# Performance work log

Hardware: AMD Instinct MI355X
Metric: run time of the kernel (lower is better)

The kernel has to match this reference:

```python
import jax, jax.numpy as jnp
import numpy as np

N_NODES = 50000
NODE_IN = 128
EDGE_IN = 16
HIDDEN = 128
N_MP = 800000
N_PRED = 400000


def setup_inputs() -> dict:
    key = jax.random.key(0)
    ks = jax.random.split(key, 12)
    s = lambda fan_in: 1.0 / np.sqrt(fan_in)
    inp = {
        'x': jax.random.normal(ks[0], (N_NODES, NODE_IN), jnp.float32),
        'mp_edge_index': jax.random.randint(ks[1], (2, N_MP), 0, N_NODES, jnp.int64),
        'pred_edge_index': jax.random.randint(ks[2], (2, N_PRED), 0, N_NODES, jnp.int64),
        'pred_edge_attr': jax.random.normal(ks[3], (N_PRED, EDGE_IN), jnp.float32),
        # SAGEConv1: lin_l (neighbors, with bias), lin_r (root, no bias)
        'W1_l': jax.random.normal(ks[4], (HIDDEN, NODE_IN), jnp.float32) * s(NODE_IN),
        'b1': jnp.zeros((HIDDEN,), jnp.float32),
        'W1_r': jax.random.normal(ks[5], (HIDDEN, NODE_IN), jnp.float32) * s(NODE_IN),
        # SAGEConv2
        'W2_l': jax.random.normal(ks[6], (HIDDEN, HIDDEN), jnp.float32) * s(HIDDEN),
        'b2': jnp.zeros((HIDDEN,), jnp.float32),
        'W2_r': jax.random.normal(ks[7], (HIDDEN, HIDDEN), jnp.float32) * s(HIDDEN),
        # edge MLP: Linear(2*H+E -> H), ReLU, Linear(H -> 1)
        'Wm1': jax.random.normal(ks[8], (HIDDEN, 2 * HIDDEN + EDGE_IN), jnp.float32) * s(2 * HIDDEN + EDGE_IN),
        'bm1': jnp.zeros((HIDDEN,), jnp.float32),
        'Wm2': jax.random.normal(ks[9], (1, HIDDEN), jnp.float32) * s(HIDDEN),
        'bm2': jnp.zeros((1,), jnp.float32),
    }
    return inp


def _sage_conv(h, src, dst, W_l, b_l, W_r, n_nodes):
    # PyG SAGEConv with mean aggregation: out_i = W_l @ mean_{j->i} h_j + b_l + W_r @ h_i
    msg_sum = jax.ops.segment_sum(h[src], dst, num_segments=n_nodes)
    deg = jax.ops.segment_sum(jnp.ones((src.shape[0],), h.dtype), dst, num_segments=n_nodes)
    mean = msg_sum / jnp.maximum(deg, 1.0)[:, None]
    return mean @ W_l.T + b_l + h @ W_r.T


def reference(x, mp_edge_index, pred_edge_index, pred_edge_attr,
              W1_l, b1, W1_r, W2_l, b2, W2_r, Wm1, bm1, Wm2, bm2):
    n = x.shape[0]
    src, dst = mp_edge_index[0], mp_edge_index[1]
    h = jax.nn.relu(_sage_conv(x, src, dst, W1_l, b1, W1_r, n))
    h = jax.nn.relu(_sage_conv(h, src, dst, W2_l, b2, W2_r, n))
    ps, pd = pred_edge_index[0], pred_edge_index[1]
    edge_repr = jnp.concatenate([h[ps], h[pd], pred_edge_attr], axis=-1)  # [E_pred, 2H+E]
    hidden = jax.nn.relu(edge_repr @ Wm1.T + bm1)
    return (hidden @ Wm2.T + bm2)[:, 0]
```

## Files before the change

kernel.cpp:

```cpp
#include <hip/hip_runtime.h>
#include <hip/hip_bf16.h>

#define HIDDEN 128

typedef __attribute__((ext_vector_type(8))) short s16x8;
typedef __attribute__((ext_vector_type(4))) short s16x4;
typedef __attribute__((ext_vector_type(4))) float f32x4;
typedef __attribute__((ext_vector_type(8))) __bf16 bf16x8;

__device__ __forceinline__ short f2bf(float x) {
    unsigned u = __float_as_uint(x);
    unsigned r = (u + 0x7fffu + ((u >> 16) & 1u)) >> 16;
    return (short)r;
}
__device__ __forceinline__ float bf2f(short s) {
    return __uint_as_float(((unsigned)(unsigned short)s) << 16);
}

__global__ void k_split(const float* __restrict__ in, short* __restrict__ hi,
                        short* __restrict__ lo, int n4) {
    int i = blockIdx.x * blockDim.x + threadIdx.x;
    if (i >= n4) return;
    float4 v = ((const float4*)in)[i];
    s16x4 h, l;
    h[0] = f2bf(v.x); l[0] = f2bf(v.x - bf2f(h[0]));
    h[1] = f2bf(v.y); l[1] = f2bf(v.y - bf2f(h[1]));
    h[2] = f2bf(v.z); l[2] = f2bf(v.z - bf2f(h[2]));
    h[3] = f2bf(v.w); l[3] = f2bf(v.w - bf2f(h[3]));
    ((s16x4*)hi)[i] = h;
    ((s16x4*)lo)[i] = l;
}

__global__ void k_packw_conv(const float* __restrict__ Wl, const float* __restrict__ Wr,
                             short* __restrict__ Bh, short* __restrict__ Bl) {
    int idx = blockIdx.x * blockDim.x + threadIdx.x;
    if (idx >= 8 * 8 * 64) return;
    int l = idx & 63;
    int t = (idx >> 6) & 7;
    int s = idx >> 9;
    int n = t * 16 + (l & 15);
    int kbase = s * 32 + (l >> 4) * 8;
    s16x8 h, lo;
    #pragma unroll
    for (int j = 0; j < 8; ++j) {
        int k = kbase + j;
        float v = (k < 128) ? Wl[n * 128 + k] : Wr[n * 128 + (k - 128)];
        short hs = f2bf(v);
        h[j] = hs;
        lo[j] = f2bf(v - bf2f(hs));
    }
    ((s16x8*)Bh)[idx] = h;
    ((s16x8*)Bl)[idx] = lo;
}

__global__ void k_packw_uv(const float* __restrict__ Wm1, short* __restrict__ Bh,
                           short* __restrict__ Bl) {
    int idx = blockIdx.x * blockDim.x + threadIdx.x;
    if (idx >= 4 * 16 * 64) return;
    int l = idx & 63;
    int t = (idx >> 6) & 15;
    int s = idx >> 10;
    int np = t * 16 + (l & 15);
    int kbase = s * 32 + (l >> 4) * 8;
    s16x8 h, lo;
    #pragma unroll
    for (int j = 0; j < 8; ++j) {
        int k = kbase + j;
        float v = (np < 128) ? Wm1[np * 272 + k] : Wm1[(np - 128) * 272 + 128 + k];
        short hs = f2bf(v);
        h[j] = hs;
        lo[j] = f2bf(v - bf2f(hs));
    }
    ((s16x8*)Bh)[idx] = h;
    ((s16x8*)Bl)[idx] = lo;
}

__global__ void k_deg(const int* __restrict__ dst, int* __restrict__ deg, int n_edges) {
    for (int e = blockIdx.x * blockDim.x + threadIdx.x; e < n_edges; e += gridDim.x * blockDim.x)
        atomicAdd(&deg[dst[e]], 1);
}

__global__ __launch_bounds__(1024) void k_scan_blk(const int* __restrict__ deg,
                                                   int* __restrict__ row_start,
                                                   int* __restrict__ part, int n) {
    __shared__ int wsum[16];
    int tid = threadIdx.x;
    int lane = tid & 63;
    int w = tid >> 6;
    int i = blockIdx.x * 1024 + tid;
    int v = (i < n) ? deg[i] : 0;
    int s = v;
    #pragma unroll
    for (int off = 1; off < 64; off <<= 1) {
        int t = __shfl_up(s, off, 64);
        if (lane >= off) s += t;
    }
    if (lane == 63) wsum[w] = s;
    __syncthreads();
    if (w == 0) {
        int ws = (lane < 16) ? wsum[lane] : 0;
        #pragma unroll
        for (int off = 1; off < 16; off <<= 1) {
            int t = __shfl_up(ws, off, 64);
            if (lane >= off) ws += t;
        }
        if (lane < 16) wsum[lane] = ws;
    }
    __syncthreads();
    int incl = s + ((w > 0) ? wsum[w - 1] : 0);
    if (i < n) row_start[i] = incl - v;
    if (tid == 1023) part[blockIdx.x] = incl;
}

__global__ void k_scan_top(int* __restrict__ part, int* __restrict__ row_start,
                           int P, int n) {
    int lane = threadIdx.x;
    int v = (lane < P) ? part[lane] : 0;
    int s = v;
    #pragma unroll
    for (int off = 1; off < 64; off <<= 1) {
        int t = __shfl_up(s, off, 64);
        if (lane >= off) s += t;
    }
    if (lane < P) part[lane] = s - v;
    if (lane == P - 1) row_start[n] = s;
}

__global__ __launch_bounds__(1024) void k_scan_add(int* __restrict__ row_start,
                                                   int* __restrict__ cursor,
                                                   const int* __restrict__ part, int n) {
    int i = blockIdx.x * 1024 + threadIdx.x;
    if (i < n) {
        int r = row_start[i] + part[blockIdx.x];
        row_start[i] = r;
        cursor[i] = r;
    }
}

__global__ void k_fill(const int* __restrict__ src, const int* __restrict__ dst,
                       int* __restrict__ cursor, int* __restrict__ csr, int n_edges) {
    for (int e = blockIdx.x * blockDim.x + threadIdx.x; e < n_edges; e += gridDim.x * blockDim.x) {
        int d = dst[e];
        int p = atomicAdd(&cursor[d], 1);
        csr[p] = src[e];
    }
}

__global__ __launch_bounds__(256) void k_agg_f32(const float* __restrict__ feat,
                                                 const int* __restrict__ row_start,
                                                 const int* __restrict__ csr,
                                                 short* __restrict__ Mh,
                                                 short* __restrict__ Ml, int n_nodes) {
    int wave = (blockIdx.x * 256 + threadIdx.x) >> 6;
    if (wave >= n_nodes) return;
    int lane = threadIdx.x & 63;
    int s = row_start[wave], e = row_start[wave + 1];
    const float2* f2p = (const float2*)feat;
    float ax = 0.f, ay = 0.f;
    for (int j = s; j < e; ++j) {
        int nb = csr[j];
        float2 v = f2p[nb * 64 + lane];
        ax += v.x; ay += v.y;
    }
    float inv = (e > s) ? 1.0f / (float)(e - s) : 0.0f;
    float m0 = ax * inv, m1 = ay * inv;
    short h0 = f2bf(m0), l0 = f2bf(m0 - bf2f(h0));
    short h1 = f2bf(m1), l1 = f2bf(m1 - bf2f(h1));
    ((ushort2*)Mh)[wave * 64 + lane] = make_ushort2((unsigned short)h0, (unsigned short)h1);
    ((ushort2*)Ml)[wave * 64 + lane] = make_ushort2((unsigned short)l0, (unsigned short)l1);
}

__global__ __launch_bounds__(256) void k_agg_sp(const short* __restrict__ Fh,
                                                const short* __restrict__ Fl,
                                                const int* __restrict__ row_start,
                                                const int* __restrict__ csr,
                                                short* __restrict__ Mh,
                                                short* __restrict__ Ml, int n_nodes) {
    int wave = (blockIdx.x * 256 + threadIdx.x) >> 6;
    if (wave >= n_nodes) return;
    int lane = threadIdx.x & 63;
    int s = row_start[wave], e = row_start[wave + 1];
    const ushort2* fh = (const ushort2*)Fh;
    const ushort2* fl = (const ushort2*)Fl;
    float ax = 0.f, ay = 0.f;
    for (int j = s; j < e; ++j) {
        int nb = csr[j];
        ushort2 qh = fh[nb * 64 + lane];
        ushort2 ql = fl[nb * 64 + lane];
        ax += bf2f((short)qh.x) + bf2f((short)ql.x);
        ay += bf2f((short)qh.y) + bf2f((short)ql.y);
    }
    float inv = (e > s) ? 1.0f / (float)(e - s) : 0.0f;
    float m0 = ax * inv, m1 = ay * inv;
    short h0 = f2bf(m0), l0 = f2bf(m0 - bf2f(h0));
    short h1 = f2bf(m1), l1 = f2bf(m1 - bf2f(h1));
    ((ushort2*)Mh)[wave * 64 + lane] = make_ushort2((unsigned short)h0, (unsigned short)h1);
    ((ushort2*)Ml)[wave * 64 + lane] = make_ushort2((unsigned short)l0, (unsigned short)l1);
}

__global__ __launch_bounds__(256, 4) void k_convm(
    const short* __restrict__ Mh, const short* __restrict__ Ml,
    const short* __restrict__ Rh, const short* __restrict__ Rl,
    const short* __restrict__ Bh, const short* __restrict__ Bl,
    const float* __restrict__ bias, short* __restrict__ Oh, short* __restrict__ Ol,
    int n_nodes) {
    __shared__ __align__(16) short Ah[32][264];
    __shared__ __align__(16) short Al[32][264];
    int tid = threadIdx.x;
    int node0 = blockIdx.x * 32;
    const s16x8* Mh8 = (const s16x8*)Mh;
    const s16x8* Ml8 = (const s16x8*)Ml;
    const s16x8* Rh8 = (const s16x8*)Rh;
    const s16x8* Rl8 = (const s16x8*)Rl;
    for (int i = tid; i < 32 * 32; i += 256) {
        int row = i >> 5, grp = i & 31;
        int node = node0 + row;
        s16x8 vh = (s16x8)0, vl = (s16x8)0;
        if (node < n_nodes) {
            vh = (grp < 16) ? Mh8[node * 16 + grp] : Rh8[node * 16 + (grp - 16)];
            vl = (grp < 16) ? Ml8[node * 16 + grp] : Rl8[node * 16 + (grp - 16)];
        }
        *(s16x8*)&Ah[row][grp * 8] = vh;
        *(s16x8*)&Al[row][grp * 8] = vl;
    }
    __syncthreads();

    int lane = tid & 63;
    int w = tid >> 6;
    int rowid = lane & 15;
    int g = lane >> 4;
    int t0 = w * 2;

    f32x4 acc[2][2];
    acc[0][0] = (f32x4)0.f; acc[0][1] = (f32x4)0.f;
    acc[1][0] = (f32x4)0.f; acc[1][1] = (f32x4)0.f;

    const bf16x8* Bh8 = (const bf16x8*)Bh;
    const bf16x8* Bl8 = (const bf16x8*)Bl;
    bf16x8 bh0 = Bh8[t0 * 64 + lane];
    bf16x8 bh1 = Bh8[(t0 + 1) * 64 + lane];
    bf16x8 bl0 = Bl8[t0 * 64 + lane];
    bf16x8 bl1 = Bl8[(t0 + 1) * 64 + lane];

    #pragma unroll
    for (int s = 0; s < 8; ++s) {
        bf16x8 nh0 = bh0, nh1 = bh1, nl0 = bl0, nl1 = bl1;
        if (s < 7) {
            nh0 = Bh8[((s + 1) * 8 + t0) * 64 + lane];
            nh1 = Bh8[((s + 1) * 8 + t0 + 1) * 64 + lane];
            nl0 = Bl8[((s + 1) * 8 + t0) * 64 + lane];
            nl1 = Bl8[((s + 1) * 8 + t0 + 1) * 64 + lane];
        }
        int kf = s * 32 + g * 8;
        bf16x8 a_h[2], a_l[2];
        #pragma unroll
        for (int m = 0; m < 2; ++m) {
            a_h[m] = *(const bf16x8*)&Ah[m * 16 + rowid][kf];
            a_l[m] = *(const bf16x8*)&Al[m * 16 + rowid][kf];
        }
        #pragma unroll
        for (int m = 0; m < 2; ++m) {
            acc[m][0] = __builtin_amdgcn_mfma_f32_16x16x32_bf16(a_h[m], bh0, acc[m][0], 0, 0, 0);
            acc[m][1] = __builtin_amdgcn_mfma_f32_16x16x32_bf16(a_h[m], bh1, acc[m][1], 0, 0, 0);
            acc[m][0] = __builtin_amdgcn_mfma_f32_16x16x32_bf16(a_l[m], bh0, acc[m][0], 0, 0, 0);
            acc[m][1] = __builtin_amdgcn_mfma_f32_16x16x32_bf16(a_l[m], bh1, acc[m][1], 0, 0, 0);
            acc[m][0] = __builtin_amdgcn_mfma_f32_16x16x32_bf16(a_h[m], bl0, acc[m][0], 0, 0, 0);
            acc[m][1] = __builtin_amdgcn_mfma_f32_16x16x32_bf16(a_h[m], bl1, acc[m][1], 0, 0, 0);
        }
        bh0 = nh0; bh1 = nh1; bl0 = nl0; bl1 = nl1;
    }

    int n0 = w * 32 + rowid;
    int n1 = n0 + 16;
    float b_0 = bias[n0], b_1 = bias[n1];
    unsigned short* OhU = (unsigned short*)Oh;
    unsigned short* OlU = (unsigned short*)Ol;
    #pragma unroll
    for (int m = 0; m < 2; ++m) {
        int node = node0 + m * 16 + g * 4;
        #pragma unroll
        for (int r = 0; r < 4; ++r) {
            if (node + r < n_nodes) {
                float v0 = fmaxf(acc[m][0][r] + b_0, 0.f);
                float v1 = fmaxf(acc[m][1][r] + b_1, 0.f);
                short h0 = f2bf(v0), l0 = f2bf(v0 - bf2f(h0));
                short h1 = f2bf(v1), l1 = f2bf(v1 - bf2f(h1));
                OhU[(node + r) * 128 + n0] = (unsigned short)h0;
                OlU[(node + r) * 128 + n0] = (unsigned short)l0;
                OhU[(node + r) * 128 + n1] = (unsigned short)h1;
                OlU[(node + r) * 128 + n1] = (unsigned short)l1;
            }
        }
    }
}

__global__ __launch_bounds__(256, 4) void k_guv(
    const short* __restrict__ H2h, const short* __restrict__ H2l,
    const short* __restrict__ Bh, const short* __restrict__ Bl,
    float* __restrict__ U, float* __restrict__ V, int n_nodes) {
    __shared__ __align__(16) short Ah[32][136];
    __shared__ __align__(16) short Al[32][136];
    int tid = threadIdx.x;
    int node0 = blockIdx.x * 32;
    const s16x8* Hh8 = (const s16x8*)H2h;
    const s16x8* Hl8 = (const s16x8*)H2l;
    for (int i = tid; i < 32 * 16; i += 256) {
        int row = i >> 4, grp = i & 15;
        int node = node0 + row;
        s16x8 vh = (s16x8)0, vl = (s16x8)0;
        if (node < n_nodes) {
            vh = Hh8[node * 16 + grp];
            vl = Hl8[node * 16 + grp];
        }
        *(s16x8*)&Ah[row][grp * 8] = vh;
        *(s16x8*)&Al[row][grp * 8] = vl;
    }
    __syncthreads();

    int lane = tid & 63;
    int w = tid >> 6;
    int rowid = lane & 15;
    int g = lane >> 4;
    int t0 = w * 4;

    f32x4 acc[2][4];
    #pragma unroll
    for (int m = 0; m < 2; ++m)
        #pragma unroll
        for (int q = 0; q < 4; ++q) acc[m][q] = (f32x4)0.f;

    const bf16x8* Bh8 = (const bf16x8*)Bh;
    const bf16x8* Bl8 = (const bf16x8*)Bl;

    #pragma unroll
    for (int s = 0; s < 4; ++s) {
        bf16x8 bh[4], bl[4];
        #pragma unroll
        for (int q = 0; q < 4; ++q) {
            bh[q] = Bh8[(s * 16 + t0 + q) * 64 + lane];
            bl[q] = Bl8[(s * 16 + t0 + q) * 64 + lane];
        }
        int kf = s * 32 + g * 8;
        bf16x8 a_h[2], a_l[2];
        #pragma unroll
        for (int m = 0; m < 2; ++m) {
            a_h[m] = *(const bf16x8*)&Ah[m * 16 + rowid][kf];
            a_l[m] = *(const bf16x8*)&Al[m * 16 + rowid][kf];
        }
        #pragma unroll
        for (int m = 0; m < 2; ++m) {
            #pragma unroll
            for (int q = 0; q < 4; ++q) {
                acc[m][q] = __builtin_amdgcn_mfma_f32_16x16x32_bf16(a_h[m], bh[q], acc[m][q], 0, 0, 0);
                acc[m][q] = __builtin_amdgcn_mfma_f32_16x16x32_bf16(a_l[m], bh[q], acc[m][q], 0, 0, 0);
                acc[m][q] = __builtin_amdgcn_mfma_f32_16x16x32_bf16(a_h[m], bl[q], acc[m][q], 0, 0, 0);
            }
        }
    }

    float* dstbase = (w < 2) ? U : V;
    int cb = (w & 1) * 64 + rowid;
    #pragma unroll
    for (int m = 0; m < 2; ++m) {
        int node = node0 + m * 16 + g * 4;
        #pragma unroll
        for (int q = 0; q < 4; ++q) {
            int col = cb + q * 16;
            #pragma unroll
            for (int r = 0; r < 4; ++r) {
                if (node + r < n_nodes)
                    dstbase[(node + r) * 128 + col] = acc[m][q][r];
            }
        }
    }
}

__global__ __launch_bounds__(256) void k_edge(
    const float* __restrict__ U, const float* __restrict__ V,
    const int* __restrict__ ps, const int* __restrict__ pd,
    const float* __restrict__ attr, const float* __restrict__ Wm1,
    const float* __restrict__ bm1, const float* __restrict__ wm2,
    const float* __restrict__ bm2, float* __restrict__ outp, int n_edges) {
    int lane = threadIdx.x & 63;
    int wid = (blockIdx.x * 256 + threadIdx.x) >> 6;
    int nw = (gridDim.x * 256) >> 6;

    int j0 = 2 * lane;
    float wa0[16], wa1[16];
    #pragma unroll
    for (int k4 = 0; k4 < 4; ++k4) {
        float4 t = *(const float4*)&Wm1[j0 * 272 + 256 + k4 * 4];
        wa0[k4 * 4 + 0] = t.x; wa0[k4 * 4 + 1] = t.y; wa0[k4 * 4 + 2] = t.z; wa0[k4 * 4 + 3] = t.w;
        float4 u = *(const float4*)&Wm1[(j0 + 1) * 272 + 256 + k4 * 4];
        wa1[k4 * 4 + 0] = u.x; wa1[k4 * 4 + 1] = u.y; wa1[k4 * 4 + 2] = u.z; wa1[k4 * 4 + 3] = u.w;
    }
    float bb0 = bm1[j0], bb1 = bm1[j0 + 1];
    float wm0 = wm2[j0], wm1v = wm2[j0 + 1];
    float bm2v = bm2[0];

    const float2* U2 = (const float2*)U;
    const float2* V2 = (const float2*)V;
    const float4* at4 = (const float4*)attr;

    for (int e = wid; e < n_edges; e += nw) {
        int s = ps[e];
        int d = pd[e];
        float2 u = U2[s * 64 + lane];
        float2 v = V2[d * 64 + lane];
        float4 a0 = at4[e * 4 + 0];
        float4 a1 = at4[e * 4 + 1];
        float4 a2 = at4[e * 4 + 2];
        float4 a3 = at4[e * 4 + 3];
        float av[16] = {a0.x, a0.y, a0.z, a0.w, a1.x, a1.y, a1.z, a1.w,
                        a2.x, a2.y, a2.z, a2.w, a3.x, a3.y, a3.z, a3.w};
        float t0 = 0.f, t1 = 0.f;
        #pragma unroll
        for (int k = 0; k < 16; ++k) {
            t0 += wa0[k] * av[k];
            t1 += wa1[k] * av[k];
        }
        float p = fmaxf(u.x + v.x + t0 + bb0, 0.f) * wm0
                + fmaxf(u.y + v.y + t1 + bb1, 0.f) * wm1v;
        p += __shfl_xor(p, 32, 64);
        p += __shfl_xor(p, 16, 64);
        p += __shfl_xor(p, 8, 64);
        p += __shfl_xor(p, 4, 64);
        p += __shfl_xor(p, 2, 64);
        p += __shfl_xor(p, 1, 64);
        if (lane == 0) outp[e] = p + bm2v;
    }
}

extern "C" void kernel_launch(void* const* d_in, const int* in_sizes, int n_in,
                              void* d_out, int out_size, void* d_ws, size_t ws_size,
                              hipStream_t stream) {
    const float* x     = (const float*)d_in[0];
    const int*   mp    = (const int*)d_in[1];
    const int*   pe    = (const int*)d_in[2];
    const float* attr  = (const float*)d_in[3];
    const float* W1_l  = (const float*)d_in[4];
    const float* b1    = (const float*)d_in[5];
    const float* W1_r  = (const float*)d_in[6];
    const float* W2_l  = (const float*)d_in[7];
    const float* b2    = (const float*)d_in[8];
    const float* W2_r  = (const float*)d_in[9];
    const float* Wm1   = (const float*)d_in[10];
    const float* bm1   = (const float*)d_in[11];
    const float* Wm2   = (const float*)d_in[12];
    const float* bm2   = (const float*)d_in[13];
    float* out = (float*)d_out;

    const int n_nodes = in_sizes[0] / HIDDEN;
    const int n_mp    = in_sizes[1] / 2;
    const int n_pred  = in_sizes[2] / 2;

    const int* mp_src = mp;
    const int* mp_dst = mp + n_mp;
    const int* p_src  = pe;
    const int* p_dst  = pe + n_pred;

    char* ws = (char*)d_ws;
    size_t off = 0;
    auto alloc = [&](size_t bytes) -> void* {
        void* p = ws + off;
        off += (bytes + 255) & ~(size_t)255;
        return p;
    };
    short* Wc1h = (short*)alloc(8 * 8 * 64 * 8 * sizeof(short));
    short* Wc1l = (short*)alloc(8 * 8 * 64 * 8 * sizeof(short));
    short* Wc2h = (short*)alloc(8 * 8 * 64 * 8 * sizeof(short));
    short* Wc2l = (short*)alloc(8 * 8 * 64 * 8 * sizeof(short));
    short* Buvh = (short*)alloc(4 * 16 * 64 * 8 * sizeof(short));
    short* Buvl = (short*)alloc(4 * 16 * 64 * 8 * sizeof(short));
    int*   deg    = (int*)alloc((size_t)n_nodes * sizeof(int));
    int*   rowst  = (int*)alloc(((size_t)n_nodes + 1) * sizeof(int));
    int*   cursor = (int*)alloc((size_t)n_nodes * sizeof(int));
    int*   part   = (int*)alloc(64 * sizeof(int));
    int*   csr    = (int*)alloc((size_t)n_mp * sizeof(int));
    short* Xh  = (short*)alloc((size_t)n_nodes * HIDDEN * sizeof(short));
    short* Xl  = (short*)alloc((size_t)n_nodes * HIDDEN * sizeof(short));
    short* Mh  = (short*)alloc((size_t)n_nodes * HIDDEN * sizeof(short));
    short* Ml  = (short*)alloc((size_t)n_nodes * HIDDEN * sizeof(short));
    short* H1h = (short*)alloc((size_t)n_nodes * HIDDEN * sizeof(short));
    short* H1l = (short*)alloc((size_t)n_nodes * HIDDEN * sizeof(short));
    short* H2h = (short*)alloc((size_t)n_nodes * HIDDEN * sizeof(short));
    short* H2l = (short*)alloc((size_t)n_nodes * HIDDEN * sizeof(short));
    float* Ubuf = (float*)alloc((size_t)n_nodes * HIDDEN * sizeof(float));
    float* Vbuf = (float*)alloc((size_t)n_nodes * HIDDEN * sizeof(float));
    (void)ws_size; (void)n_in; (void)out_size;

    const int P = (n_nodes + 1023) / 1024;

    hipMemsetAsync(deg, 0, (size_t)n_nodes * sizeof(int), stream);

    k_packw_conv<<<16, 256, 0, stream>>>(W1_l, W1_r, Wc1h, Wc1l);
    k_packw_conv<<<16, 256, 0, stream>>>(W2_l, W2_r, Wc2h, Wc2l);
    k_packw_uv<<<16, 256, 0, stream>>>(Wm1, Buvh, Buvl);
    k_split<<<(n_nodes * 32 + 255) / 256, 256, 0, stream>>>(x, Xh, Xl, n_nodes * 32);

    k_deg<<<(n_mp + 255) / 256, 256, 0, stream>>>(mp_dst, deg, n_mp);
    k_scan_blk<<<P, 1024, 0, stream>>>(deg, rowst, part, n_nodes);
    k_scan_top<<<1, 64, 0, stream>>>(part, rowst, P, n_nodes);
    k_scan_add<<<P, 1024, 0, stream>>>(rowst, cursor, part, n_nodes);
    k_fill<<<(n_mp + 255) / 256, 256, 0, stream>>>(mp_src, mp_dst, cursor, csr, n_mp);

    k_agg_f32<<<(n_nodes + 3) / 4, 256, 0, stream>>>(x, rowst, csr, Mh, Ml, n_nodes);
    k_convm<<<(n_nodes + 31) / 32, 256, 0, stream>>>(Mh, Ml, Xh, Xl, Wc1h, Wc1l, b1,
                                                     H1h, H1l, n_nodes);
    k_agg_sp<<<(n_nodes + 3) / 4, 256, 0, stream>>>(H1h, H1l, rowst, csr, Mh, Ml, n_nodes);
    k_convm<<<(n_nodes + 31) / 32, 256, 0, stream>>>(Mh, Ml, H1h, H1l, Wc2h, Wc2l, b2,
                                                     H2h, H2l, n_nodes);

    k_guv<<<(n_nodes + 31) / 32, 256, 0, stream>>>(H2h, H2l, Buvh, Buvl, Ubuf, Vbuf, n_nodes);
    k_edge<<<2048, 256, 0, stream>>>(Ubuf, Vbuf, p_src, p_dst, attr, Wm1,
                                     bm1, Wm2, bm2, out, n_pred);
}
```

Measured before the change: 550.1 us.

## Fuse prep kernels, unroll neighbor aggregation, split hi/lo lanes, two edges per wave

Merges the memset, three weight-pack kernels and the x split into one launch, removing several small launches and their gaps. The aggregation loops are unrolled by two so each wave has two neighbor gathers in flight. The second aggregation has half the wave read hi and half read lo in 4-wide vectors, combined with a cross-half shuffle. The edge kernel handles two edges per wave iteration and adds an occupancy hint, which gives more memory parallelism at the cost of more registers.

```diff
diff --git a/kernel.cpp b/kernel.cpp
--- a/kernel.cpp
+++ b/kernel.cpp
@@ -17,24 +17,10 @@
     return __uint_as_float(((unsigned)(unsigned short)s) << 16);
 }
 
-__global__ void k_split(const float* __restrict__ in, short* __restrict__ hi,
-                        short* __restrict__ lo, int n4) {
-    int i = blockIdx.x * blockDim.x + threadIdx.x;
-    if (i >= n4) return;
-    float4 v = ((const float4*)in)[i];
-    s16x4 h, l;
-    h[0] = f2bf(v.x); l[0] = f2bf(v.x - bf2f(h[0]));
-    h[1] = f2bf(v.y); l[1] = f2bf(v.y - bf2f(h[1]));
-    h[2] = f2bf(v.z); l[2] = f2bf(v.z - bf2f(h[2]));
-    h[3] = f2bf(v.w); l[3] = f2bf(v.w - bf2f(h[3]));
-    ((s16x4*)hi)[i] = h;
-    ((s16x4*)lo)[i] = l;
-}
-
-__global__ void k_packw_conv(const float* __restrict__ Wl, const float* __restrict__ Wr,
-                             short* __restrict__ Bh, short* __restrict__ Bl) {
-    int idx = blockIdx.x * blockDim.x + threadIdx.x;
-    if (idx >= 8 * 8 * 64) return;
+__device__ __forceinline__ void pack_conv_body(const float* __restrict__ Wl,
+                                               const float* __restrict__ Wr,
+                                               short* __restrict__ Bh,
+                                               short* __restrict__ Bl, int idx) {
     int l = idx & 63;
     int t = (idx >> 6) & 7;
     int s = idx >> 9;
@@ -53,10 +39,9 @@
     ((s16x8*)Bl)[idx] = lo;
 }
 
-__global__ void k_packw_uv(const float* __restrict__ Wm1, short* __restrict__ Bh,
-                           short* __restrict__ Bl) {
-    int idx = blockIdx.x * blockDim.x + threadIdx.x;
-    if (idx >= 4 * 16 * 64) return;
+__device__ __forceinline__ void pack_uv_body(const float* __restrict__ Wm1,
+                                             short* __restrict__ Bh,
+                                             short* __restrict__ Bl, int idx) {
     int l = idx & 63;
     int t = (idx >> 6) & 15;
     int s = idx >> 10;
@@ -73,6 +58,41 @@
     }
     ((s16x8*)Bh)[idx] = h;
     ((s16x8*)Bl)[idx] = lo;
+}
+
+__global__ void k_prep(const float* __restrict__ x,
+                       const float* __restrict__ W1_l, const float* __restrict__ W1_r,
+                       const float* __restrict__ W2_l, const float* __restrict__ W2_r,
+                       const float* __restrict__ Wm1,
+                       short* __restrict__ Wc1h, short* __restrict__ Wc1l,
+                       short* __restrict__ Wc2h, short* __restrict__ Wc2l,
+                       short* __restrict__ Buvh, short* __restrict__ Buvl,
+                       short* __restrict__ Xh, short* __restrict__ Xl,
+                       int* __restrict__ deg, int n_nodes, int degb, int nsplit4) {
+    int b = blockIdx.x;
+    int tid = threadIdx.x;
+    if (b < 16) {
+        pack_conv_body(W1_l, W1_r, Wc1h, Wc1l, b * 256 + tid);
+    } else if (b < 32) {
+        pack_conv_body(W2_l, W2_r, Wc2h, Wc2l, (b - 16) * 256 + tid);
+    } else if (b < 48) {
+        pack_uv_body(Wm1, Buvh, Buvl, (b - 32) * 256 + tid);
+    } else if (b < 48 + degb) {
+        int i = (b - 48) * 256 + tid;
+        if (i < n_nodes) deg[i] = 0;
+    } else {
+        int i = (b - 48 - degb) * 256 + tid;
+        if (i < nsplit4) {
+            float4 v = ((const float4*)x)[i];
+            s16x4 h, l;
+            h[0] = f2bf(v.x); l[0] = f2bf(v.x - bf2f(h[0]));
+            h[1] = f2bf(v.y); l[1] = f2bf(v.y - bf2f(h[1]));
+            h[2] = f2bf(v.z); l[2] = f2bf(v.z - bf2f(h[2]));
+            h[3] = f2bf(v.w); l[3] = f2bf(v.w - bf2f(h[3]));
+            ((s16x4*)Xh)[i] = h;
+            ((s16x4*)Xl)[i] = l;
+        }
+    }
 }
 
 __global__ void k_deg(const int* __restrict__ dst, int* __restrict__ deg, int n_edges) {
@@ -157,9 +177,18 @@
     int s = row_start[wave], e = row_start[wave + 1];
     const float2* f2p = (const float2*)feat;
     float ax = 0.f, ay = 0.f;
-    for (int j = s; j < e; ++j) {
+    int j = s;
+    for (; j + 1 < e; j += 2) {
+        int nb0 = csr[j];
+        int nb1 = csr[j + 1];
+        float2 v0 = f2p[(size_t)nb0 * 64 + lane];
+        float2 v1 = f2p[(size_t)nb1 * 64 + lane];
+        ax += v0.x + v1.x;
+        ay += v0.y + v1.y;
+    }
+    if (j < e) {
         int nb = csr[j];
-        float2 v = f2p[nb * 64 + lane];
+        float2 v = f2p[(size_t)nb * 64 + lane];
         ax += v.x; ay += v.y;
     }
     float inv = (e > s) ? 1.0f / (float)(e - s) : 0.0f;
@@ -179,23 +208,44 @@
     int wave = (blockIdx.x * 256 + threadIdx.x) >> 6;
     if (wave >= n_nodes) return;
     int lane = threadIdx.x & 63;
+    int half = lane >> 5;
+    int l32 = lane & 31;
+    const s16x4* base = (const s16x4*)(half ? Fl : Fh);
     int s = row_start[wave], e = row_start[wave + 1];
-    const ushort2* fh = (const ushort2*)Fh;
-    const ushort2* fl = (const ushort2*)Fl;
-    float ax = 0.f, ay = 0.f;
-    for (int j = s; j < e; ++j) {
+    float a0 = 0.f, a1 = 0.f, a2 = 0.f, a3 = 0.f;
+    int j = s;
+    for (; j + 1 < e; j += 2) {
+        int nb0 = csr[j];
+        int nb1 = csr[j + 1];
+        s16x4 q0 = base[(size_t)nb0 * 32 + l32];
+        s16x4 q1 = base[(size_t)nb1 * 32 + l32];
+        a0 += bf2f(q0[0]) + bf2f(q1[0]);
+        a1 += bf2f(q0[1]) + bf2f(q1[1]);
+        a2 += bf2f(q0[2]) + bf2f(q1[2]);
+        a3 += bf2f(q0[3]) + bf2f(q1[3]);
+    }
+    if (j < e) {
         int nb = csr[j];
-        ushort2 qh = fh[nb * 64 + lane];
-        ushort2 ql = fl[nb * 64 + lane];
-        ax += bf2f((short)qh.x) + bf2f((short)ql.x);
-        ay += bf2f((short)qh.y) + bf2f((short)ql.y);
-    }
+        s16x4 q = base[(size_t)nb * 32 + l32];
+        a0 += bf2f(q[0]); a1 += bf2f(q[1]); a2 += bf2f(q[2]); a3 += bf2f(q[3]);
+    }
+    a0 += __shfl_xor(a0, 32, 64);
+    a1 += __shfl_xor(a1, 32, 64);
+    a2 += __shfl_xor(a2, 32, 64);
+    a3 += __shfl_xor(a3, 32, 64);
     float inv = (e > s) ? 1.0f / (float)(e - s) : 0.0f;
-    float m0 = ax * inv, m1 = ay * inv;
-    short h0 = f2bf(m0), l0 = f2bf(m0 - bf2f(h0));
-    short h1 = f2bf(m1), l1 = f2bf(m1 - bf2f(h1));
-    ((ushort2*)Mh)[wave * 64 + lane] = make_ushort2((unsigned short)h0, (unsigned short)h1);
-    ((ushort2*)Ml)[wave * 64 + lane] = make_ushort2((unsigned short)l0, (unsigned short)l1);
+    float m0 = a0 * inv, m1 = a1 * inv, m2 = a2 * inv, m3 = a3 * inv;
+    short h0 = f2bf(m0), h1 = f2bf(m1), h2 = f2bf(m2), h3 = f2bf(m3);
+    s16x4 o;
+    if (half == 0) {
+        o[0] = h0; o[1] = h1; o[2] = h2; o[3] = h3;
+    } else {
+        o[0] = f2bf(m0 - bf2f(h0));
+        o[1] = f2bf(m1 - bf2f(h1));
+        o[2] = f2bf(m2 - bf2f(h2));
+        o[3] = f2bf(m3 - bf2f(h3));
+    }
+    ((s16x4*)(half ? Ml : Mh))[(size_t)wave * 32 + l32] = o;
 }
 
 __global__ __launch_bounds__(256, 4) void k_convm(
@@ -375,7 +425,7 @@
     }
 }
 
-__global__ __launch_bounds__(256) void k_edge(
+__global__ __launch_bounds__(256, 4) void k_edge(
     const float* __restrict__ U, const float* __restrict__ V,
     const int* __restrict__ ps, const int* __restrict__ pd,
     const float* __restrict__ attr, const float* __restrict__ Wm1,
@@ -386,48 +436,71 @@
     int nw = (gridDim.x * 256) >> 6;
 
     int j0 = 2 * lane;
-    float wa0[16], wa1[16];
-    #pragma unroll
-    for (int k4 = 0; k4 < 4; ++k4) {
-        float4 t = *(const float4*)&Wm1[j0 * 272 + 256 + k4 * 4];
-        wa0[k4 * 4 + 0] = t.x; wa0[k4 * 4 + 1] = t.y; wa0[k4 * 4 + 2] = t.z; wa0[k4 * 4 + 3] = t.w;
-        float4 u = *(const float4*)&Wm1[(j0 + 1) * 272 + 256 + k4 * 4];
-        wa1[k4 * 4 + 0] = u.x; wa1[k4 * 4 + 1] = u.y; wa1[k4 * 4 + 2] = u.z; wa1[k4 * 4 + 3] = u.w;
-    }
+    const float* wr0 = &Wm1[j0 * 272 + 256];
+    const float* wr1 = &Wm1[(j0 + 1) * 272 + 256];
+    float4 wa0a = *(const float4*)&wr0[0];
+    float4 wa0b = *(const float4*)&wr0[4];
+    float4 wa0c = *(const float4*)&wr0[8];
+    float4 wa0d = *(const float4*)&wr0[12];
+    float4 wa1a = *(const float4*)&wr1[0];
+    float4 wa1b = *(const float4*)&wr1[4];
+    float4 wa1c = *(const float4*)&wr1[8];
+    float4 wa1d = *(const float4*)&wr1[12];
     float bb0 = bm1[j0], bb1 = bm1[j0 + 1];
-    float wm0 = wm2[j0], wm1v = wm2[j0 + 1];
+    float wm0 = wm2[j0], wmv1 = wm2[j0 + 1];
     float bm2v = bm2[0];
 
     const float2* U2 = (const float2*)U;
     const float2* V2 = (const float2*)V;
     const float4* at4 = (const float4*)attr;
 
-    for (int e = wid; e < n_edges; e += nw) {
-        int s = ps[e];
-        int d = pd[e];
-        float2 u = U2[s * 64 + lane];
-        float2 v = V2[d * 64 + lane];
-        float4 a0 = at4[e * 4 + 0];
-        float4 a1 = at4[e * 4 + 1];
-        float4 a2 = at4[e * 4 + 2];
-        float4 a3 = at4[e * 4 + 3];
-        float av[16] = {a0.x, a0.y, a0.z, a0.w, a1.x, a1.y, a1.z, a1.w,
-                        a2.x, a2.y, a2.z, a2.w, a3.x, a3.y, a3.z, a3.w};
-        float t0 = 0.f, t1 = 0.f;
-        #pragma unroll
-        for (int k = 0; k < 16; ++k) {
-            t0 += wa0[k] * av[k];
-            t1 += wa1[k] * av[k];
-        }
-        float p = fmaxf(u.x + v.x + t0 + bb0, 0.f) * wm0
-                + fmaxf(u.y + v.y + t1 + bb1, 0.f) * wm1v;
-        p += __shfl_xor(p, 32, 64);
-        p += __shfl_xor(p, 16, 64);
-        p += __shfl_xor(p, 8, 64);
-        p += __shfl_xor(p, 4, 64);
-        p += __shfl_xor(p, 2, 64);
-        p += __shfl_xor(p, 1, 64);
-        if (lane == 0) outp[e] = p + bm2v;
+    for (int e = wid * 2; e < n_edges; e += 2 * nw) {
+        int e1 = e + 1;
+        bool has1 = (e1 < n_edges);
+        int e1c = has1 ? e1 : e;
+        int s0 = ps[e],   d0 = pd[e];
+        int s1 = ps[e1c], d1 = pd[e1c];
+        float2 u0 = U2[(size_t)s0 * 64 + lane];
+        float2 v0 = V2[(size_t)d0 * 64 + lane];
+        float2 u1 = U2[(size_t)s1 * 64 + lane];
+        float2 v1 = V2[(size_t)d1 * 64 + lane];
+        float4 a00 = at4[(size_t)e * 4 + 0];
+        float4 a01 = at4[(size_t)e * 4 + 1];
+        float4 a02 = at4[(size_t)e * 4 + 2];
+        float4 a03 = at4[(size_t)e * 4 + 3];
+        float4 a10 = at4[(size_t)e1c * 4 + 0];
+        float4 a11 = at4[(size_t)e1c * 4 + 1];
+        float4 a12 = at4[(size_t)e1c * 4 + 2];
+        float4 a13 = at4[(size_t)e1c * 4 + 3];
+
+        float t00 = wa0a.x * a00.x + wa0a.y * a00.y + wa0a.z * a00.z + wa0a.w * a00.w
+                  + wa0b.x * a01.x + wa0b.y * a01.y + wa0b.z * a01.z + wa0b.w * a01.w
+                  + wa0c.x * a02.x + wa0c.y * a02.y + wa0c.z * a02.z + wa0c.w * a02.w
+                  + wa0d.x * a03.x + wa0d.y * a03.y + wa0d.z * a03.z + wa0d.w * a03.w;
+        float t01 = wa1a.x * a00.x + wa1a.y * a00.y + wa1a.z * a00.z + wa1a.w * a00.w
+                  + wa1b.x * a01.x + wa1b.y * a01.y + wa1b.z * a01.z + wa1b.w * a01.w
+                  + wa1c.x * a02.x + wa1c.y * a02.y + wa1c.z * a02.z + wa1c.w * a02.w
+                  + wa1d.x * a03.x + wa1d.y * a03.y + wa1d.z * a03.z + wa1d.w * a03.w;
+        float t10 = wa0a.x * a10.x + wa0a.y * a10.y + wa0a.z * a10.z + wa0a.w * a10.w
+                  + wa0b.x * a11.x + wa0b.y * a11.y + wa0b.z * a11.z + wa0b.w * a11.w
+                  + wa0c.x * a12.x + wa0c.y * a12.y + wa0c.z * a12.z + wa0c.w * a12.w
+                  + wa0d.x * a13.x + wa0d.y * a13.y + wa0d.z * a13.z + wa0d.w * a13.w;
+        float t11 = wa1a.x * a10.x + wa1a.y * a10.y + wa1a.z * a10.z + wa1a.w * a10.w
+                  + wa1b.x * a11.x + wa1b.y * a11.y + wa1b.z * a11.z + wa1b.w * a11.w
+                  + wa1c.x * a12.x + wa1c.y * a12.y + wa1c.z * a12.z + wa1c.w * a12.w
+                  + wa1d.x * a13.x + wa1d.y * a13.y + wa1d.z * a13.z + wa1d.w * a13.w;
+
+        float p0 = fmaxf(u0.x + v0.x + t00 + bb0, 0.f) * wm0
+                 + fmaxf(u0.y + v0.y + t01 + bb1, 0.f) * wmv1;
+        float p1 = fmaxf(u1.x + v1.x + t10 + bb0, 0.f) * wm0
+                 + fmaxf(u1.y + v1.y + t11 + bb1, 0.f) * wmv1;
+        #pragma unroll
+        for (int m = 32; m >= 1; m >>= 1) {
+            p0 += __shfl_xor(p0, m, 64);
+            p1 += __shfl_xor(p1, m, 64);
+        }
+        if (lane == 0) outp[e] = p0 + bm2v;
+        if (lane == 1 && has1) outp[e1] = p1 + bm2v;
     }
 }
 
@@ -490,13 +563,13 @@
     (void)ws_size; (void)n_in; (void)out_size;
 
     const int P = (n_nodes + 1023) / 1024;
-
-    hipMemsetAsync(deg, 0, (size_t)n_nodes * sizeof(int), stream);
-
-    k_packw_conv<<<16, 256, 0, stream>>>(W1_l, W1_r, Wc1h, Wc1l);
-    k_packw_conv<<<16, 256, 0, stream>>>(W2_l, W2_r, Wc2h, Wc2l);
-    k_packw_uv<<<16, 256, 0, stream>>>(Wm1, Buvh, Buvl);
-    k_split<<<(n_nodes * 32 + 255) / 256, 256, 0, stream>>>(x, Xh, Xl, n_nodes * 32);
+    const int degb = (n_nodes + 255) / 256;
+    const int nsplit4 = n_nodes * 32;
+    const int splitb = (nsplit4 + 255) / 256;
+
+    k_prep<<<48 + degb + splitb, 256, 0, stream>>>(x, W1_l, W1_r, W2_l, W2_r, Wm1,
+                                                   Wc1h, Wc1l, Wc2h, Wc2l, Buvh, Buvl,
+                                                   Xh, Xl, deg, n_nodes, degb, nsplit4);
 
     k_deg<<<(n_mp + 255) / 256, 256, 0, stream>>>(mp_dst, deg, n_mp);
     k_scan_blk<<<P, 1024, 0, stream>>>(deg, rowst, part, n_nodes);
```

Measured after the change: 607.7 us. 10.5% more time.
